# Kernel optimization log

Measured on AMD Instinct MI355X. Metric: run time of the kernel, lower is better.

## Reference

```python
import jax, jax.numpy as jnp
import numpy as np

B, N, K, DIM = 1, 50000, 16, 64


def setup_inputs() -> dict:
    key = jax.random.key(0)
    ks = jax.random.split(key, 16)
    s = 0.05  # weight init scale
    return {
        "points_xyz": jax.random.normal(ks[0], (B, N, 3), jnp.float32),
        "points_features": jax.random.normal(ks[1], (B, N, DIM), jnp.float32),
        "neighbours_xyz": jax.random.normal(ks[2], (B, N, K, 3), jnp.float32),
        "neighbours_features": jax.random.normal(ks[3], (B, N, K, DIM), jnp.float32),
        "W_phi": jax.random.normal(ks[4], (DIM, DIM), jnp.float32) * s,
        "b_phi": jnp.zeros((DIM,), jnp.float32),
        "W_psi": jax.random.normal(ks[5], (DIM, DIM), jnp.float32) * s,
        "b_psi": jnp.zeros((DIM,), jnp.float32),
        "W_alpha": jax.random.normal(ks[6], (DIM, DIM), jnp.float32) * s,
        "b_alpha": jnp.zeros((DIM,), jnp.float32),
        "W_gamma": jax.random.normal(ks[7], (DIM, DIM), jnp.float32) * s,
        "b_gamma": jnp.zeros((DIM,), jnp.float32),
        "W_d1": jax.random.normal(ks[8], (3, DIM), jnp.float32) * s,
        "b_d1": jnp.zeros((DIM,), jnp.float32),
        "W_d2": jax.random.normal(ks[9], (DIM, DIM), jnp.float32) * s,
        "b_d2": jnp.zeros((DIM,), jnp.float32),
    }


def reference(points_xyz, points_features, neighbours_xyz, neighbours_features,
              W_phi, b_phi, W_psi, b_psi, W_alpha, b_alpha, W_gamma, b_gamma,
              W_d1, b_d1, W_d2, b_d2):
    # Positional encoding: delta(p_i - p_j) -> (B, N, K, DIM)
    diff = points_xyz[:, :, None, :] - neighbours_xyz          # (B,N,K,3)
    delta = jax.nn.relu((diff @ W_d1 + b_d1) @ W_d2 + b_d2)    # (B,N,K,DIM)

    phi = (points_features @ W_phi + b_phi)[:, :, None, :]     # (B,N,1,DIM)
    psi = neighbours_features @ W_psi + b_psi                  # (B,N,K,DIM)
    beta = phi - psi + delta                                   # (B,N,K,DIM)

    gamma_out = beta @ W_gamma + b_gamma                       # (B,N,K,DIM)
    # NOTE: faithful to source: softmax over the FEATURE axis (dim=-1)
    rho = jax.nn.softmax(gamma_out, axis=-1)                   # (B,N,K,DIM)

    alpha_out = neighbours_features @ W_alpha + b_alpha + delta  # (B,N,K,DIM)
    out = jnp.sum(rho * alpha_out, axis=2)                     # (B,N,DIM)
    return out
```

## Files before the change

kernel.cpp:

```cpp
#include <hip/hip_runtime.h>
#include <hip/hip_bf16.h>

typedef unsigned int uint_t;
typedef __attribute__((ext_vector_type(8))) short bf16x8;
typedef __attribute__((ext_vector_type(4))) float f32x4;

#define NPTS 50000
#define DIM  64
#define KNB  16
#define GPW  8
#define NGROUPS (NPTS / GPW)
#define WPB  4
#define NBLOCKS ((NGROUPS + WPB - 1) / WPB)

#define FR_WA    0
#define FR_PSIG  2048
#define FR_WG    4096
#define FR_PHIG  6144
#define WC4      8192
#define GB       8448
#define BA       8512

__device__ __forceinline__ uint_t pk(float a, float b) {
    union { __hip_bfloat162 h; uint_t u; } cv;
    cv.h = __float22bfloat162_rn(float2{a, b});
    return cv.u;
}

union Frag { uint_t u[4]; bf16x8 s; uint4 v; };

__device__ __forceinline__ int sigma(int k) {
    int t = k >> 1;
    return (t & 15) + 32 * (t >> 4) + 16 * (k & 1);
}

__global__ void pt_prep(const float* __restrict__ Wphi, const float* __restrict__ bphi,
                        const float* __restrict__ Wpsi, const float* __restrict__ bpsi,
                        const float* __restrict__ Wa,   const float* __restrict__ ba,
                        const float* __restrict__ Wg,   const float* __restrict__ bg,
                        const float* __restrict__ Wd1,  const float* __restrict__ bd1,
                        const float* __restrict__ Wd2,  const float* __restrict__ bd2,
                        float* __restrict__ ws) {
    int b = blockIdx.x, t = threadIdx.x;
    uint_t* wsu = (uint_t*)ws;
    if (b < 32) {
        int gid  = b * 256 + t;
        int img  = gid >> 11;
        int rem  = gid & 2047;
        int f    = rem >> 8;
        int lane = (rem >> 2) & 63;
        int w    = rem & 3;
        int k0   = (f & 1) * 32 + (lane >> 4) * 8 + 2 * w;
        int k1   = k0 + 1;
        int n    = (f >> 1) * 16 + (lane & 15);
        float v0, v1;
        if (img == 0) {
            v0 = Wa[k0 * 64 + n]; v1 = Wa[k1 * 64 + n];
            wsu[FR_WA + rem] = pk(v0, v1);
        } else if (img == 1) {
            float a0 = 0.f, a1 = 0.f;
            for (int c = 0; c < 64; ++c) {
                float wgc = Wg[c * 64 + n];
                a0 += Wpsi[k0 * 64 + c] * wgc;
                a1 += Wpsi[k1 * 64 + c] * wgc;
            }
            wsu[FR_PSIG + rem] = pk(-a0, -a1);
        } else if (img == 2) {
            v0 = Wg[sigma(k0) * 64 + n]; v1 = Wg[sigma(k1) * 64 + n];
            wsu[FR_WG + rem] = pk(v0, v1);
        } else {
            float a0 = 0.f, a1 = 0.f;
            for (int c = 0; c < 64; ++c) {
                float wgc = Wg[c * 64 + n];
                a0 += Wphi[k0 * 64 + c] * wgc;
                a1 += Wphi[k1 * 64 + c] * wgc;
            }
            wsu[FR_PHIG + rem] = pk(a0, a1);
        }
    } else if (t < 64) {
        float wx = 0.f, wy = 0.f, wz = 0.f;
        for (int m = 0; m < 64; ++m) {
            float w2 = Wd2[m * 64 + t];
            wx += Wd1[m] * w2;
            wy += Wd1[64 + m] * w2;
            wz += Wd1[128 + m] * w2;
        }
        float wb = bd2[t];
        for (int m = 0; m < 64; ++m) wb += bd1[m] * Wd2[m * 64 + t];
        ws[WC4 + t * 4 + 0] = wx;
        ws[WC4 + t * 4 + 1] = wy;
        ws[WC4 + t * 4 + 2] = wz;
        ws[WC4 + t * 4 + 3] = wb;
        float g = bg[t];
        for (int c = 0; c < 64; ++c) g += (bphi[c] - bpsi[c]) * Wg[c * 64 + t];
        ws[GB + t] = g;
        ws[BA + t] = ba[t];
    }
}

#define MFMA(A, B, C) __builtin_amdgcn_mfma_f32_16x16x32_bf16((A), (B), (C), 0, 0, 0)

#define WAREA 1224

__global__ __launch_bounds__(256, 2)
void pt_main(const float* __restrict__ pxyz, const float* __restrict__ pfeat,
             const float* __restrict__ nxyz, const float* __restrict__ nfeat,
             const float* __restrict__ ws,   float* __restrict__ out) {
    __shared__ float lds[WPB][WAREA];

    const int t    = threadIdx.x;
    const int wv   = t >> 6;
    const int lane = t & 63;
    const int c16  = lane & 15;
    const int quad = lane >> 4;

    const int g = blockIdx.x * WPB + wv;
    if (g >= NGROUPS) return;

    float*  phig_s = &lds[wv][0];
    uint_t* utr    = (uint_t*)(phig_s + 520);
    float*  dxyz   = (float*)(utr + 544);
    float*  pxyz_s = dxyz + 128;

    const uint4* fr = (const uint4*)ws;
    Frag wa[8], wpsig[8], wg[8];
    #pragma unroll
    for (int f = 0; f < 8; ++f) {
        wa[f].v    = fr[           f * 64 + lane];
        wpsig[f].v = fr[ 512 +     f * 64 + lane];
        wg[f].v    = fr[1024 +     f * 64 + lane];
    }
    float4 wc[4];
    float ba_r[4], gbr[4];
    #pragma unroll
    for (int nt = 0; nt < 4; ++nt) {
        int d = nt * 16 + c16;
        wc[nt]   = ((const float4*)(ws + WC4))[d];
        ba_r[nt] = ws[BA + d];
        gbr[nt]  = ws[GB + d];
    }

    const int g0 = g * GPW;
    const int k3 = lane / 3, c3 = lane - k3 * 3;

    if (lane < 24) pxyz_s[lane] = pxyz[g0 * 3 + lane];
    float nv0 = (lane < 48) ? nxyz[(size_t)g0 * 48 + lane] : 0.f;
    if (lane < 48) dxyz[k3 * 4 + c3] = pxyz_s[c3] - nv0;

    {
        float4 x0{}, x1{}, x2{}, x3{};
        if (c16 < 8) {
            const float* base = pfeat + (size_t)(g0 + c16) * 64 + quad * 8;
            x0 = *(const float4*)(base);
            x1 = *(const float4*)(base + 4);
            x2 = *(const float4*)(base + 32);
            x3 = *(const float4*)(base + 36);
        }
        Frag pa0, pa1;
        pa0.u[0] = pk(x0.x, x0.y); pa0.u[1] = pk(x0.z, x0.w);
        pa0.u[2] = pk(x1.x, x1.y); pa0.u[3] = pk(x1.z, x1.w);
        pa1.u[0] = pk(x2.x, x2.y); pa1.u[1] = pk(x2.z, x2.w);
        pa1.u[2] = pk(x3.x, x3.y); pa1.u[3] = pk(x3.z, x3.w);
        #pragma unroll
        for (int nt = 0; nt < 4; ++nt) {
            Frag b0, b1;
            b0.v = fr[1536 + (nt * 2 + 0) * 64 + lane];
            b1.v = fr[1536 + (nt * 2 + 1) * 64 + lane];
            f32x4 acc = {gbr[nt], gbr[nt], gbr[nt], gbr[nt]};
            acc = MFMA(pa0.s, b0.s, acc);
            acc = MFMA(pa1.s, b1.s, acc);
            if (quad < 2) {
                #pragma unroll
                for (int r = 0; r < 4; ++r)
                    phig_s[(quad * 4 + r) * 65 + nt * 16 + c16] = acc[r];
            }
        }
    }

    const float* nfb = nfeat + (size_t)g0 * (KNB * 64) + (size_t)c16 * 64 + quad * 8;
    float4 f0 = *(const float4*)(nfb);
    float4 f1 = *(const float4*)(nfb + 4);
    float4 f2 = *(const float4*)(nfb + 32);
    float4 f3 = *(const float4*)(nfb + 36);
    float nvn = (lane < 48) ? nxyz[(size_t)g0 * 48 + 48 + lane] : 0.f;

    #pragma unroll 1
    for (int i = 0; i < GPW; ++i) {
        const int n = g0 + i;

        Frag na0, na1;
        na0.u[0] = pk(f0.x, f0.y); na0.u[1] = pk(f0.z, f0.w);
        na0.u[2] = pk(f1.x, f1.y); na0.u[3] = pk(f1.z, f1.w);
        na1.u[0] = pk(f2.x, f2.y); na1.u[1] = pk(f2.z, f2.w);
        na1.u[2] = pk(f3.x, f3.y); na1.u[3] = pk(f3.z, f3.w);
        if (i + 1 < GPW) {
            const float* nf2 = nfb + (size_t)(i + 1) * (KNB * 64);
            f0 = *(const float4*)(nf2);
            f1 = *(const float4*)(nf2 + 4);
            f2 = *(const float4*)(nf2 + 32);
            f3 = *(const float4*)(nf2 + 36);
        }

        float ph[4];
        #pragma unroll
        for (int nt = 0; nt < 4; ++nt) ph[nt] = phig_s[i * 65 + nt * 16 + c16];
        float4 dd[4];
        #pragma unroll
        for (int r = 0; r < 4; ++r)
            dd[r] = ((const float4*)dxyz)[(i & 1) * 16 + quad * 4 + r];

        if (i + 1 < GPW) {
            if (lane < 48)
                dxyz[((i + 1) & 1) * 64 + k3 * 4 + c3] = pxyz_s[(i + 1) * 3 + c3] - nvn;
            if (i + 2 < GPW)
                nvn = (lane < 48) ? nxyz[((size_t)n + 2) * 48 + lane] : 0.f;
        }

        float d_c[4][4];
        #pragma unroll
        for (int nt = 0; nt < 4; ++nt) {
            #pragma unroll
            for (int r = 0; r < 4; ++r) {
                float u = fmaf(dd[r].x, wc[nt].x,
                          fmaf(dd[r].y, wc[nt].y,
                          fmaf(dd[r].z, wc[nt].z, wc[nt].w)));
                d_c[nt][r] = fmaxf(u, 0.f);
            }
        }
        #pragma unroll
        for (int r = 0; r < 4; ++r) {
            int row = (quad * 4 + r) * 34;
            utr[row + c16]      = pk(d_c[0][r], d_c[1][r]);
            utr[row + 16 + c16] = pk(d_c[2][r], d_c[3][r]);
        }

        f32x4 aacc[4];
        #pragma unroll
        for (int nt = 0; nt < 4; ++nt) {
            aacc[nt] = f32x4{ba_r[nt], ba_r[nt], ba_r[nt], ba_r[nt]};
            aacc[nt] = MFMA(na0.s, wa[nt * 2 + 0].s, aacc[nt]);
            aacc[nt] = MFMA(na1.s, wa[nt * 2 + 1].s, aacc[nt]);
        }
        f32x4 gacc[4];
        #pragma unroll
        for (int nt = 0; nt < 4; ++nt) {
            gacc[nt] = f32x4{ph[nt], ph[nt], ph[nt], ph[nt]};
            gacc[nt] = MFMA(na0.s, wpsig[nt * 2 + 0].s, gacc[nt]);
            gacc[nt] = MFMA(na1.s, wpsig[nt * 2 + 1].s, gacc[nt]);
        }
        Frag da0, da1;
        {
            const uint_t* rowp = utr + c16 * 34 + quad * 4;
            uint2 a = *(const uint2*)(rowp);
            uint2 b = *(const uint2*)(rowp + 2);
            uint2 c = *(const uint2*)(rowp + 16);
            uint2 d = *(const uint2*)(rowp + 18);
            da0.u[0] = a.x; da0.u[1] = a.y; da0.u[2] = b.x; da0.u[3] = b.y;
            da1.u[0] = c.x; da1.u[1] = c.y; da1.u[2] = d.x; da1.u[3] = d.y;
        }
        #pragma unroll
        for (int nt = 0; nt < 4; ++nt) {
            gacc[nt] = MFMA(da0.s, wg[nt * 2 + 0].s, gacc[nt]);
            gacc[nt] = MFMA(da1.s, wg[nt * 2 + 1].s, gacc[nt]);
        }
        #pragma unroll
        for (int nt = 0; nt < 4; ++nt)
            #pragma unroll
            for (int r = 0; r < 4; ++r) aacc[nt][r] += d_c[nt][r];

        float e[4][4], smi[4];
        #pragma unroll
        for (int r = 0; r < 4; ++r) {
            float s = 0.f;
            #pragma unroll
            for (int nt = 0; nt < 4; ++nt) { e[nt][r] = __expf(gacc[nt][r]); s += e[nt][r]; }
            #pragma unroll
            for (int d2 = 1; d2 < 16; d2 <<= 1) s += __shfl_xor(s, d2);
            smi[r] = __builtin_amdgcn_rcpf(s);
        }
        float p0 = 0.f, p1 = 0.f, p2 = 0.f, p3 = 0.f;
        #pragma unroll
        for (int r = 0; r < 4; ++r) {
            p0 = fmaf(e[0][r] * smi[r], aacc[0][r], p0);
            p1 = fmaf(e[1][r] * smi[r], aacc[1][r], p1);
            p2 = fmaf(e[2][r] * smi[r], aacc[2][r], p2);
            p3 = fmaf(e[3][r] * smi[r], aacc[3][r], p3);
        }
        p0 += __shfl_xor(p0, 16); p0 += __shfl_xor(p0, 32);
        p1 += __shfl_xor(p1, 16); p1 += __shfl_xor(p1, 32);
        p2 += __shfl_xor(p2, 16); p2 += __shfl_xor(p2, 32);
        p3 += __shfl_xor(p3, 16); p3 += __shfl_xor(p3, 32);
        float sel = (quad == 0) ? p0 : (quad == 1) ? p1 : (quad == 2) ? p2 : p3;
        out[(size_t)n * 64 + lane] = sel;
    }
}

extern "C" void kernel_launch(void* const* d_in, const int* in_sizes, int n_in,
                              void* d_out, int out_size, void* d_ws, size_t ws_size,
                              hipStream_t stream) {
    const float* pxyz  = (const float*)d_in[0];
    const float* pfeat = (const float*)d_in[1];
    const float* nxyz  = (const float*)d_in[2];
    const float* nfeat = (const float*)d_in[3];
    const float* Wphi  = (const float*)d_in[4];
    const float* bphi  = (const float*)d_in[5];
    const float* Wpsi  = (const float*)d_in[6];
    const float* bpsi  = (const float*)d_in[7];
    const float* Wa    = (const float*)d_in[8];
    const float* ba    = (const float*)d_in[9];
    const float* Wg    = (const float*)d_in[10];
    const float* bg    = (const float*)d_in[11];
    const float* Wd1   = (const float*)d_in[12];
    const float* bd1   = (const float*)d_in[13];
    const float* Wd2   = (const float*)d_in[14];
    const float* bd2   = (const float*)d_in[15];
    float* ws = (float*)d_ws;

    pt_prep<<<33, 256, 0, stream>>>(Wphi, bphi, Wpsi, bpsi, Wa, ba, Wg, bg,
                                    Wd1, bd1, Wd2, bd2, ws);
    pt_main<<<NBLOCKS, 256, 0, stream>>>(pxyz, pfeat, nxyz, nfeat, ws, (float*)d_out);
}
```

Before: 347.1 us.

## Stage MFMA weight fragments in LDS and prefetch two points ahead

Moves the 24 weight fragments per lane (96 VGPRs) out of registers into a block-shared LDS copy loaded once per block. Each MFMA reloads its fragment from LDS, which frees registers so launch bounds can rise to 3 blocks per CU. The point loop is unrolled by two so neighbour features are prefetched two points ahead. This adds LDS traffic and a block-wide sync, and the extra occupancy and deeper prefetch are meant to hide global load latency.

Measured after the change: 358.9 us. 1.03x slower.

```diff
diff --git a/kernel.cpp b/kernel.cpp
--- a/kernel.cpp
+++ b/kernel.cpp
@@ -102,10 +102,11 @@
 
 #define WAREA 1224
 
-__global__ __launch_bounds__(256, 2)
+__global__ __launch_bounds__(256, 3)
 void pt_main(const float* __restrict__ pxyz, const float* __restrict__ pfeat,
              const float* __restrict__ nxyz, const float* __restrict__ nfeat,
              const float* __restrict__ ws,   float* __restrict__ out) {
+    __shared__ uint4 wfr[1536];
     __shared__ float lds[WPB][WAREA];
 
     const int t    = threadIdx.x;
@@ -114,6 +115,11 @@
     const int c16  = lane & 15;
     const int quad = lane >> 4;
 
+    const uint4* fr = (const uint4*)ws;
+
+    for (int idx = t; idx < 1536; idx += 256) wfr[idx] = fr[idx];
+    __syncthreads();
+
     const int g = blockIdx.x * WPB + wv;
     if (g >= NGROUPS) return;
 
@@ -122,14 +128,6 @@
     float*  dxyz   = (float*)(utr + 544);
     float*  pxyz_s = dxyz + 128;
 
-    const uint4* fr = (const uint4*)ws;
-    Frag wa[8], wpsig[8], wg[8];
-    #pragma unroll
-    for (int f = 0; f < 8; ++f) {
-        wa[f].v    = fr[           f * 64 + lane];
-        wpsig[f].v = fr[ 512 +     f * 64 + lane];
-        wg[f].v    = fr[1024 +     f * 64 + lane];
-    }
     float4 wc[4];
     float ba_r[4], gbr[4];
     #pragma unroll
@@ -178,28 +176,38 @@
     }
 
     const float* nfb = nfeat + (size_t)g0 * (KNB * 64) + (size_t)c16 * 64 + quad * 8;
-    float4 f0 = *(const float4*)(nfb);
-    float4 f1 = *(const float4*)(nfb + 4);
-    float4 f2 = *(const float4*)(nfb + 32);
-    float4 f3 = *(const float4*)(nfb + 36);
+    float4 pf0[4], pf1[4];
+    pf0[0] = *(const float4*)(nfb);
+    pf0[1] = *(const float4*)(nfb + 4);
+    pf0[2] = *(const float4*)(nfb + 32);
+    pf0[3] = *(const float4*)(nfb + 36);
+    {
+        const float* nf1 = nfb + (KNB * 64);
+        pf1[0] = *(const float4*)(nf1);
+        pf1[1] = *(const float4*)(nf1 + 4);
+        pf1[2] = *(const float4*)(nf1 + 32);
+        pf1[3] = *(const float4*)(nf1 + 36);
+    }
     float nvn = (lane < 48) ? nxyz[(size_t)g0 * 48 + 48 + lane] : 0.f;
 
-    #pragma unroll 1
-    for (int i = 0; i < GPW; ++i) {
+    auto do_point = [&](int i, float4 (&pf)[4]) {
         const int n = g0 + i;
 
         Frag na0, na1;
-        na0.u[0] = pk(f0.x, f0.y); na0.u[1] = pk(f0.z, f0.w);
-        na0.u[2] = pk(f1.x, f1.y); na0.u[3] = pk(f1.z, f1.w);
-        na1.u[0] = pk(f2.x, f2.y); na1.u[1] = pk(f2.z, f2.w);
-        na1.u[2] = pk(f3.x, f3.y); na1.u[3] = pk(f3.z, f3.w);
-        if (i + 1 < GPW) {
-            const float* nf2 = nfb + (size_t)(i + 1) * (KNB * 64);
-            f0 = *(const float4*)(nf2);
-            f1 = *(const float4*)(nf2 + 4);
-            f2 = *(const float4*)(nf2 + 32);
-            f3 = *(const float4*)(nf2 + 36);
-        }
+        na0.u[0] = pk(pf[0].x, pf[0].y); na0.u[1] = pk(pf[0].z, pf[0].w);
+        na0.u[2] = pk(pf[1].x, pf[1].y); na0.u[3] = pk(pf[1].z, pf[1].w);
+        na1.u[0] = pk(pf[2].x, pf[2].y); na1.u[1] = pk(pf[2].z, pf[2].w);
+        na1.u[2] = pk(pf[3].x, pf[3].y); na1.u[3] = pk(pf[3].z, pf[3].w);
+        if (i + 2 < GPW) {
+            const float* nf2 = nfb + (size_t)(i + 2) * (KNB * 64);
+            pf[0] = *(const float4*)(nf2);
+            pf[1] = *(const float4*)(nf2 + 4);
+            pf[2] = *(const float4*)(nf2 + 32);
+            pf[3] = *(const float4*)(nf2 + 36);
+        }
+
+        uint_t woff = 0;
+        asm volatile("" : "+v"(woff));
 
         float ph[4];
         #pragma unroll
@@ -237,17 +245,28 @@
         f32x4 aacc[4];
         #pragma unroll
         for (int nt = 0; nt < 4; ++nt) {
+            Frag b0, b1;
+            b0.v = wfr[woff + (nt * 2 + 0) * 64 + lane];
+            b1.v = wfr[woff + (nt * 2 + 1) * 64 + lane];
             aacc[nt] = f32x4{ba_r[nt], ba_r[nt], ba_r[nt], ba_r[nt]};
-            aacc[nt] = MFMA(na0.s, wa[nt * 2 + 0].s, aacc[nt]);
-            aacc[nt] = MFMA(na1.s, wa[nt * 2 + 1].s, aacc[nt]);
+            aacc[nt] = MFMA(na0.s, b0.s, aacc[nt]);
+            aacc[nt] = MFMA(na1.s, b1.s, aacc[nt]);
         }
         f32x4 gacc[4];
         #pragma unroll
         for (int nt = 0; nt < 4; ++nt) {
+            Frag b0, b1;
+            b0.v = wfr[woff + 512 + (nt * 2 + 0) * 64 + lane];
+            b1.v = wfr[woff + 512 + (nt * 2 + 1) * 64 + lane];
             gacc[nt] = f32x4{ph[nt], ph[nt], ph[nt], ph[nt]};
-            gacc[nt] = MFMA(na0.s, wpsig[nt * 2 + 0].s, gacc[nt]);
-            gacc[nt] = MFMA(na1.s, wpsig[nt * 2 + 1].s, gacc[nt]);
-        }
+            gacc[nt] = MFMA(na0.s, b0.s, gacc[nt]);
+            gacc[nt] = MFMA(na1.s, b1.s, gacc[nt]);
+        }
+        #pragma unroll
+        for (int nt = 0; nt < 4; ++nt)
+            #pragma unroll
+            for (int r = 0; r < 4; ++r) aacc[nt][r] += d_c[nt][r];
+
         Frag da0, da1;
         {
             const uint_t* rowp = utr + c16 * 34 + quad * 4;
@@ -260,13 +279,12 @@
         }
         #pragma unroll
         for (int nt = 0; nt < 4; ++nt) {
-            gacc[nt] = MFMA(da0.s, wg[nt * 2 + 0].s, gacc[nt]);
-            gacc[nt] = MFMA(da1.s, wg[nt * 2 + 1].s, gacc[nt]);
-        }
-        #pragma unroll
-        for (int nt = 0; nt < 4; ++nt)
-            #pragma unroll
-            for (int r = 0; r < 4; ++r) aacc[nt][r] += d_c[nt][r];
+            Frag b0, b1;
+            b0.v = wfr[woff + 1024 + (nt * 2 + 0) * 64 + lane];
+            b1.v = wfr[woff + 1024 + (nt * 2 + 1) * 64 + lane];
+            gacc[nt] = MFMA(da0.s, b0.s, gacc[nt]);
+            gacc[nt] = MFMA(da1.s, b1.s, gacc[nt]);
+        }
 
         float e[4][4], smi[4];
         #pragma unroll
@@ -292,6 +310,12 @@
         p3 += __shfl_xor(p3, 16); p3 += __shfl_xor(p3, 32);
         float sel = (quad == 0) ? p0 : (quad == 1) ? p1 : (quad == 2) ? p2 : p3;
         out[(size_t)n * 64 + lane] = sel;
+    };
+
+    #pragma unroll 1
+    for (int ii = 0; ii < GPW / 2; ++ii) {
+        do_point(2 * ii,     pf0);
+        do_point(2 * ii + 1, pf1);
     }
 }
 
```
